# Kernel tuning notes

Measured on AMD Instinct MI355X. Metric: run time of the kernel, lower is better.

## Reference

```python
import jax, jax.numpy as jnp
import numpy as np

LAMBDA_REG = 50.0  # default lambda_reg of MetaOptNetHead_Ridge


def setup_inputs() -> dict:
    key = jax.random.key(0)
    k1, k2, k3 = jax.random.split(key, 3)
    T, NQ, NS, D, NWAY, NSHOT = 256, 300, 25, 640, 5, 5
    query = jax.random.normal(k1, (T, NQ, D), dtype=jnp.float32)
    support = jax.random.normal(k2, (T, NS, D), dtype=jnp.float32)
    support_labels = jax.random.randint(k3, (T, NS), 0, NWAY)
    scale = jnp.ones((1,), dtype=jnp.float32)  # learned scale of ClassificationHead
    return {"query": query, "support": support, "scale": scale,
            "support_labels": support_labels, "n_way": NWAY, "n_shot": NSHOT}


def reference(query, support, scale, support_labels, n_way, n_shot):
    # query: (T, NQ, D), support: (T, NS, D), support_labels: (T, NS) int
    T, NS, D = support.shape
    # Linear-kernel Gram matrix with ridge regularizer: K = S S^T + lambda I, per task
    K = jnp.einsum('tnd,tmd->tnm', support, support)
    K = K + LAMBDA_REG * jnp.eye(NS, dtype=support.dtype)  # (T, NS, NS)
    # One-hot support labels (T, NS, W)
    Y = jax.nn.one_hot(support_labels, n_way, dtype=support.dtype)
    # The QPFunction in MetaOptNetHead_Ridge has zero inequality constraints
    # (C=0, h=0) and no equality constraints, so the optimum is the
    # unconstrained stationary point: x = -G^{-1} e = 2 K^{-1} Y (batched over
    # task; the n_way block-repeat of G corresponds to the W columns of Y).
    X = 2.0 * jnp.linalg.solve(K, Y)  # (T, NS, W) dual solution qp_sol
    # compatibility = support @ query^T : (T, NS, NQ); logits = sum_s compat * qp_sol
    compat = jnp.einsum('tsd,tqd->tsq', support, query)
    logits = jnp.einsum('tsq,tsw->tqw', compat, X)  # (T, NQ, W)
    return scale * logits
```

## Files before the change

kernel.cpp:

```cpp
#include <hip/hip_runtime.h>

constexpr int T_TASKS = 256;
constexpr int NQ      = 300;
constexpr int NS      = 25;
constexpr int D       = 640;
constexpr int NWAY    = 5;
constexpr float LAMBDA_REG = 50.0f;

constexpr int SP4 = 161;
constexpr int NT  = 1024;
constexpr int AC  = NS + NWAY;

__device__ __constant__ int PA[15] = {0,0,0,0,0,1,1,1,1,2,2,2,3,3,4};
__device__ __constant__ int PB[15] = {0,1,2,3,4,1,2,3,4,2,3,4,3,4,4};

__global__ __launch_bounds__(NT) void fused_ridge_head_kernel(
    const float* __restrict__ query,
    const float* __restrict__ support,
    const float* __restrict__ scale,
    const int*   __restrict__ labels,
    float*       __restrict__ out)
{
    __shared__ __align__(16) float4 sS4[NS * SP4];
    __shared__ __align__(16) float  sW[NWAY][D];
    __shared__ float aug[NS][32];
    __shared__ float sX[NS][NWAY];

    const int t   = blockIdx.x;
    const int tid = threadIdx.x;
    const float* Sg    = support + (size_t)t * NS * D;
    const float* Qbase = query   + (size_t)t * NQ * D;

    for (int idx = tid; idx < NS * 160; idx += NT) {
        int s = idx / 160, f = idx % 160;
        sS4[s * SP4 + f] = reinterpret_cast<const float4*>(Sg)[idx];
    }
    if (tid >= 960) {
        for (int idx = tid - 960; idx < NS * NWAY; idx += 64) {
            int s = idx / NWAY, w = idx % NWAY;
            aug[s][NS + w] = (labels[t * NS + s] == w) ? 2.0f : 0.0f;
        }
    }
    __syncthreads();

    if (tid < 240) {
        const int grp = tid >> 4, l = tid & 15;
        const int ra = PA[grp] * 5, rb = PB[grp] * 5;
        float acc[25] = {};
        #pragma unroll
        for (int k = 0; k < 10; ++k) {
            const int f = l + 16 * k;
            float4 A[5], B[5];
            #pragma unroll
            for (int r = 0; r < 5; ++r) A[r] = sS4[(ra + r) * SP4 + f];
            #pragma unroll
            for (int r = 0; r < 5; ++r) B[r] = sS4[(rb + r) * SP4 + f];
            #pragma unroll
            for (int i = 0; i < 5; ++i)
                #pragma unroll
                for (int j = 0; j < 5; ++j)
                    acc[i * 5 + j] += A[i].x * B[j].x + A[i].y * B[j].y +
                                      A[i].z * B[j].z + A[i].w * B[j].w;
        }
        #pragma unroll
        for (int p = 0; p < 25; ++p) {
            #pragma unroll
            for (int off = 8; off >= 1; off >>= 1)
                acc[p] += __shfl_xor(acc[p], off);
        }
        if (l == 0) {
            #pragma unroll
            for (int p = 0; p < 25; ++p) {
                int i = ra + p / 5, j = rb + p % 5;
                float v = acc[p] + (i == j ? LAMBDA_REG : 0.0f);
                aug[i][j] = v;
                aug[j][i] = v;
            }
        }
    }
    __syncthreads();

    const int g  = tid >> 4;
    const int l4 = tid & 15;
    const float4* Qp0 = reinterpret_cast<const float4*>(Qbase + (size_t)g * D);
    float4 pf0 = Qp0[l4];
    float4 pf1 = Qp0[16 + l4];

    if (tid < 64) {
        const int  c      = tid;
        const bool active = (c < AC);
        float a[NS];
        #pragma unroll
        for (int r = 0; r < NS; ++r) a[r] = active ? aug[r][c] : 0.0f;
        #pragma unroll
        for (int k = 0; k < NS; ++k) {
            float piv = __shfl(a[k], k);
            float inv = 1.0f / piv;
            a[k] *= inv;
            #pragma unroll
            for (int r = 0; r < NS; ++r) {
                if (r != k) {
                    float m = __shfl(a[r], k);
                    a[r] -= m * a[k];
                }
            }
        }
        if (active && c >= NS) {
            const int w = c - NS;
            #pragma unroll
            for (int s = 0; s < NS; ++s) sX[s][w] = a[s];
        }
    }
    __syncthreads();

    if (tid < D) {
        const float* sSf = reinterpret_cast<const float*>(sS4);
        float acc[NWAY] = {};
        #pragma unroll
        for (int s = 0; s < NS; ++s) {
            float sv = sSf[s * (SP4 * 4) + tid];
            #pragma unroll
            for (int w = 0; w < NWAY; ++w) acc[w] += sv * sX[s][w];
        }
        #pragma unroll
        for (int w = 0; w < NWAY; ++w) sW[w][tid] = acc[w];
    }
    __syncthreads();

    const float sc = scale[0];

    auto fma_step = [&](float acc[NWAY], float4 v, int i) {
        const int dbase = i * 64 + 4 * l4;
        #pragma unroll
        for (int w = 0; w < NWAY; ++w) {
            const float4 wv = *reinterpret_cast<const float4*>(&sW[w][dbase]);
            acc[w] += v.x * wv.x + v.y * wv.y + v.z * wv.z + v.w * wv.w;
        }
    };
    auto reduce_store = [&](float acc[NWAY], int q) {
        #pragma unroll
        for (int w = 0; w < NWAY; ++w) {
            #pragma unroll
            for (int off = 8; off >= 1; off >>= 1)
                acc[w] += __shfl_xor(acc[w], off);
        }
        if (l4 == 0) {
            float* o = out + ((size_t)t * NQ + q) * NWAY;
            #pragma unroll
            for (int w = 0; w < NWAY; ++w) o[w] = sc * acc[w];
        }
    };

    {
        float acc[NWAY] = {};
        fma_step(acc, pf0, 0);
        fma_step(acc, pf1, 1);
        #pragma unroll
        for (int i = 2; i < 10; ++i) fma_step(acc, Qp0[i * 16 + l4], i);
        reduce_store(acc, g);
    }
    #pragma unroll
    for (int j = 1; j < 5; ++j) {
        const int q = j * 64 + g;
        if (q < NQ) {
            const float4* Qp = reinterpret_cast<const float4*>(Qbase + (size_t)q * D);
            float acc[NWAY] = {};
            #pragma unroll
            for (int i = 0; i < 10; ++i) fma_step(acc, Qp[i * 16 + l4], i);
            reduce_store(acc, q);
        }
    }
}

extern "C" void kernel_launch(void* const* d_in, const int* in_sizes, int n_in,
                              void* d_out, int out_size, void* d_ws, size_t ws_size,
                              hipStream_t stream) {
    const float* query   = (const float*)d_in[0];
    const float* support = (const float*)d_in[1];
    const float* scale   = (const float*)d_in[2];
    const int*   labels  = (const int*)d_in[3];
    float* out = (float*)d_out;

    fused_ridge_head_kernel<<<T_TASKS, NT, 0, stream>>>(query, support, scale, labels, out);
}
```

Before: 47.97 us.

## Fuse W computation into solver warp and batch all five query rows per thread

Result: slower. 119.1 us (+148.3%).

```diff
diff --git a/kernel.cpp b/kernel.cpp
--- a/kernel.cpp
+++ b/kernel.cpp
@@ -24,12 +24,12 @@
     __shared__ __align__(16) float4 sS4[NS * SP4];
     __shared__ __align__(16) float  sW[NWAY][D];
     __shared__ float aug[NS][32];
-    __shared__ float sX[NS][NWAY];
 
     const int t   = blockIdx.x;
     const int tid = threadIdx.x;
     const float* Sg    = support + (size_t)t * NS * D;
     const float* Qbase = query   + (size_t)t * NQ * D;
+    const float sc = scale[0];
 
     for (int idx = tid; idx < NS * 160; idx += NT) {
         int s = idx / 160, f = idx % 160;
@@ -82,9 +82,14 @@
 
     const int g  = tid >> 4;
     const int l4 = tid & 15;
-    const float4* Qp0 = reinterpret_cast<const float4*>(Qbase + (size_t)g * D);
-    float4 pf0 = Qp0[l4];
-    float4 pf1 = Qp0[16 + l4];
+    const float4* Qb4 = reinterpret_cast<const float4*>(Qbase);
+    int off[5];
+    #pragma unroll
+    for (int j = 0; j < 5; ++j) {
+        int q  = g + 64 * j;
+        int qc = q < NQ ? q : NQ - 1;
+        off[j] = qc * 160 + l4;
+    }
 
     if (tid < 64) {
         const int  c      = tid;
@@ -105,70 +110,90 @@
                 }
             }
         }
-        if (active && c >= NS) {
-            const int w = c - NS;
-            #pragma unroll
-            for (int s = 0; s < NS; ++s) sX[s][w] = a[s];
-        }
-    }
+        const float* sSf = reinterpret_cast<const float*>(sS4);
+        float accw[NWAY][10];
+        #pragma unroll
+        for (int w = 0; w < NWAY; ++w)
+            #pragma unroll
+            for (int ii = 0; ii < 10; ++ii) accw[w][ii] = 0.0f;
+        #pragma unroll
+        for (int s = 0; s < NS; ++s) {
+            float X0 = __shfl(a[s], NS + 0);
+            float X1 = __shfl(a[s], NS + 1);
+            float X2 = __shfl(a[s], NS + 2);
+            float X3 = __shfl(a[s], NS + 3);
+            float X4 = __shfl(a[s], NS + 4);
+            #pragma unroll
+            for (int ii = 0; ii < 10; ++ii) {
+                float sv = sSf[s * (SP4 * 4) + c + 64 * ii];
+                accw[0][ii] += sv * X0;
+                accw[1][ii] += sv * X1;
+                accw[2][ii] += sv * X2;
+                accw[3][ii] += sv * X3;
+                accw[4][ii] += sv * X4;
+            }
+        }
+        #pragma unroll
+        for (int w = 0; w < NWAY; ++w)
+            #pragma unroll
+            for (int ii = 0; ii < 10; ++ii)
+                sW[w][c + 64 * ii] = accw[w][ii];
+    }
+
+    float4 pf0[5], pf1[5];
+    #pragma unroll
+    for (int j = 0; j < 5; ++j) pf0[j] = Qb4[off[j]];
+    #pragma unroll
+    for (int j = 0; j < 5; ++j) pf1[j] = Qb4[off[j] + 16];
+
     __syncthreads();
 
-    if (tid < D) {
-        const float* sSf = reinterpret_cast<const float*>(sS4);
-        float acc[NWAY] = {};
-        #pragma unroll
-        for (int s = 0; s < NS; ++s) {
-            float sv = sSf[s * (SP4 * 4) + tid];
-            #pragma unroll
-            for (int w = 0; w < NWAY; ++w) acc[w] += sv * sX[s][w];
-        }
-        #pragma unroll
-        for (int w = 0; w < NWAY; ++w) sW[w][tid] = acc[w];
-    }
-    __syncthreads();
-
-    const float sc = scale[0];
-
-    auto fma_step = [&](float acc[NWAY], float4 v, int i) {
+    float acc[5][NWAY];
+    #pragma unroll
+    for (int j = 0; j < 5; ++j)
+        #pragma unroll
+        for (int w = 0; w < NWAY; ++w) acc[j][w] = 0.0f;
+
+    #pragma unroll
+    for (int i = 0; i < 10; ++i) {
+        float4 qv[5];
+        if (i == 0) {
+            #pragma unroll
+            for (int j = 0; j < 5; ++j) qv[j] = pf0[j];
+        } else if (i == 1) {
+            #pragma unroll
+            for (int j = 0; j < 5; ++j) qv[j] = pf1[j];
+        } else {
+            #pragma unroll
+            for (int j = 0; j < 5; ++j) qv[j] = Qb4[off[j] + i * 16];
+        }
         const int dbase = i * 64 + 4 * l4;
         #pragma unroll
         for (int w = 0; w < NWAY; ++w) {
             const float4 wv = *reinterpret_cast<const float4*>(&sW[w][dbase]);
-            acc[w] += v.x * wv.x + v.y * wv.y + v.z * wv.z + v.w * wv.w;
-        }
-    };
-    auto reduce_store = [&](float acc[NWAY], int q) {
+            #pragma unroll
+            for (int j = 0; j < 5; ++j)
+                acc[j][w] += qv[j].x * wv.x + qv[j].y * wv.y +
+                             qv[j].z * wv.z + qv[j].w * wv.w;
+        }
+    }
+
+    #pragma unroll
+    for (int j = 0; j < 5; ++j) {
         #pragma unroll
         for (int w = 0; w < NWAY; ++w) {
             #pragma unroll
-            for (int off = 8; off >= 1; off >>= 1)
-                acc[w] += __shfl_xor(acc[w], off);
-        }
-        if (l4 == 0) {
-            float* o = out + ((size_t)t * NQ + q) * NWAY;
-            #pragma unroll
-            for (int w = 0; w < NWAY; ++w) o[w] = sc * acc[w];
-        }
-    };
-
-    {
-        float acc[NWAY] = {};
-        fma_step(acc, pf0, 0);
-        fma_step(acc, pf1, 1);
-        #pragma unroll
-        for (int i = 2; i < 10; ++i) fma_step(acc, Qp0[i * 16 + l4], i);
-        reduce_store(acc, g);
-    }
-    #pragma unroll
-    for (int j = 1; j < 5; ++j) {
-        const int q = j * 64 + g;
-        if (q < NQ) {
-            const float4* Qp = reinterpret_cast<const float4*>(Qbase + (size_t)q * D);
-            float acc[NWAY] = {};
-            #pragma unroll
-            for (int i = 0; i < 10; ++i) fma_step(acc, Qp[i * 16 + l4], i);
-            reduce_store(acc, q);
-        }
+            for (int off2 = 8; off2 >= 1; off2 >>= 1)
+                acc[j][w] += __shfl_xor(acc[j][w], off2);
+        }
+        const int q = g + 64 * j;
+        float ov = acc[j][0];
+        ov = (l4 == 1) ? acc[j][1] : ov;
+        ov = (l4 == 2) ? acc[j][2] : ov;
+        ov = (l4 == 3) ? acc[j][3] : ov;
+        ov = (l4 == 4) ? acc[j][4] : ov;
+        if (q < NQ && l4 < NWAY)
+            out[((size_t)t * NQ + q) * NWAY + l4] = sc * ov;
     }
 }
 
```
